# Kernel optimization log

Hardware: AMD Instinct MI355X
Metric: run time of the kernel (lower is better)

## Reference

```python
import jax, jax.numpy as jnp
import numpy as np

PAD_IDX = 0
VOCAB = 60
HIDDEN = 128
BATCH = 1024
SEQ = 256


def setup_inputs() -> dict:
    key = jax.random.key(0)
    ks = jax.random.split(key, 6)
    x = jax.random.randint(ks[0], (BATCH, SEQ), 0, VOCAB, dtype=jnp.int64 if jax.config.jax_enable_x64 else jnp.int32)
    lengths = jax.random.randint(ks[1], (BATCH,), 1, SEQ + 1, dtype=x.dtype)
    emb = jax.random.normal(ks[2], (VOCAB, HIDDEN), dtype=jnp.float32) * 0.1
    emb = emb.at[PAD_IDX].set(0.0)  # nn.Embedding padding_idx row is zero
    W_ih = jax.random.normal(ks[3], (HIDDEN, HIDDEN), dtype=jnp.float32) * (1.0 / np.sqrt(HIDDEN))
    W_hh = jax.random.normal(ks[4], (HIDDEN, HIDDEN), dtype=jnp.float32) * (1.0 / np.sqrt(HIDDEN))
    W_fc = jax.random.normal(ks[5], (VOCAB, HIDDEN), dtype=jnp.float32) * (1.0 / np.sqrt(HIDDEN))
    b_fc = jnp.zeros((VOCAB,), dtype=jnp.float32)
    return {"x": x, "lengths": lengths, "emb": emb, "W_ih": W_ih,
            "W_hh": W_hh, "W_fc": W_fc, "b_fc": b_fc}


def reference(x, lengths, emb, W_ih, W_hh, W_fc, b_fc):
    embedded = emb[x]                      # [B, T, H]
    B = embedded.shape[0]
    h0 = jnp.zeros((B, HIDDEN), dtype=embedded.dtype)

    def step(h_prev, x_t):
        # z_t = x_t @ W_ih^T + h_prev @ W_hh^T ; h_t = tanh(z_t)
        h_t = jnp.tanh(x_t @ W_ih.T + h_prev @ W_hh.T)
        return h_t, h_t

    _, hs = jax.lax.scan(step, h0, jnp.swapaxes(embedded, 0, 1))  # hs: [T, B, H]
    outputs = jnp.swapaxes(hs, 0, 1)       # [B, T, H]
    last_out = jnp.take_along_axis(outputs, (lengths - 1)[:, None, None], axis=1)[:, 0, :]  # [B, H]
    return last_out @ W_fc.T + b_fc[None, :]
```

## Files before the change

kernel.cpp:

```cpp
#include <hip/hip_runtime.h>
#include <hip/hip_bf16.h>

#define BATCH 1024
#define SEQ 256
#define HIDDEN 128
#define VOCAB 60
#define ROWS 4
#define CHUNK 16
#define ASTRIDE 144
#define RSTR 136

typedef _Float16 f16x8 __attribute__((ext_vector_type(8)));
typedef _Float16 f16x4 __attribute__((ext_vector_type(4)));
typedef float f32x4 __attribute__((ext_vector_type(4)));

__device__ __forceinline__ float fast_tanh(float x) {
    float e = __builtin_amdgcn_exp2f(x * 2.8853900817779268f);
    return __builtin_fmaf(-2.0f, __builtin_amdgcn_rcpf(e + 1.0f), 1.0f);
}

__global__ void rnn_prep_embw(const float* __restrict__ emb,
                              const float* __restrict__ W_ih,
                              float* __restrict__ embW) {
    const int v = blockIdx.x;
    const int i = threadIdx.x;
    __shared__ __align__(16) float e[HIDDEN];
    e[i] = emb[v * HIDDEN + i];
    __syncthreads();
    const float4* wrow = (const float4*)(W_ih + i * HIDDEN);
    const float4* e4 = (const float4*)e;
    float a0 = 0.f, a1 = 0.f, a2 = 0.f, a3 = 0.f;
#pragma unroll
    for (int j = 0; j < HIDDEN / 4; ++j) {
        float4 w = wrow[j];
        float4 h = e4[j];
        a0 += w.x * h.x; a1 += w.y * h.y; a2 += w.z * h.z; a3 += w.w * h.w;
    }
    embW[v * HIDDEN + i] = (a0 + a1) + (a2 + a3);
}

__global__ void __launch_bounds__(512)
rnn_mfma(const int* __restrict__ x, const int* __restrict__ lengths,
         const float* __restrict__ embW, const float* __restrict__ W_hh,
         const float* __restrict__ W_fc, const float* __restrict__ b_fc,
         float* __restrict__ out) {
    const int tid = threadIdx.x;
    const int wave = tid >> 6;
    const int lane = tid & 63;
    const int q = lane >> 4;
    const int r16 = lane & 15;
    const int r4 = r16 & 3;
    const int c0 = wave * 16;
    const int b0 = blockIdx.x * ROWS;

    __shared__ __align__(16) float ring[CHUNK][ROWS][RSTR];
    __shared__ __align__(16) _Float16 Ah[2][ROWS][ASTRIDE];
    __shared__ int xs[ROWS][SEQ + 1];
    __shared__ __align__(16) float hfin[ROWS][HIDDEN];
    __shared__ int lenbuf[ROWS];

    for (int idx = tid; idx < ROWS * SEQ; idx += 512) {
        int r = idx >> 8, t = idx & (SEQ - 1);
        xs[r][t] = x[(b0 + r) * SEQ + t];
    }
    if (tid < ROWS) lenbuf[tid] = lengths[b0 + tid];
    for (int idx = tid; idx < (int)(sizeof(Ah) / 4); idx += 512)
        ((int*)Ah)[idx] = 0;

    f16x8 Wf[4];
    {
        const float* wrow = W_hh + (c0 + r16) * HIDDEN + q * 8;
#pragma unroll
        for (int kc = 0; kc < 4; ++kc) {
            const float* p = wrow + kc * 32;
#pragma unroll
            for (int j = 0; j < 8; ++j) Wf[kc][j] = (_Float16)p[j];
        }
    }

    __syncthreads();

    const int mylen = lenbuf[r4];
    int lenmax = 0;
#pragma unroll
    for (int r = 0; r < ROWS; ++r) lenmax = max(lenmax, lenbuf[r]);

    const int s_c4 = tid & 31;
    const int s_r = (tid >> 5) & 3;
    const int s_tp = tid >> 7;

    f32x4 rg[4];
#pragma unroll
    for (int k = 0; k < 4; ++k) {
        int tp = s_tp + 4 * k;
        int tok = xs[s_r][tp];
        rg[k] = *(const f32x4*)(embW + tok * HIDDEN + s_c4 * 4);
    }

    int cur = 0;
    f32x4 cap = {0.f, 0.f, 0.f, 0.f};

    for (int t0 = 0; t0 < lenmax; t0 += CHUNK) {
#pragma unroll
        for (int k = 0; k < 4; ++k)
            *(f32x4*)&ring[s_tp + 4 * k][s_r][s_c4 * 4] = rg[k];
        __syncthreads();

        if (t0 + CHUNK < lenmax) {
            const int t0n = t0 + CHUNK;
#pragma unroll
            for (int k = 0; k < 4; ++k) {
                int tp = s_tp + 4 * k;
                int tok = xs[s_r][t0n + tp];
                rg[k] = *(const f32x4*)(embW + tok * HIDDEN + s_c4 * 4);
            }
        }

        const int tend = (lenmax - t0 < CHUNK) ? lenmax - t0 : CHUNK;
        for (int tt = 0; tt < tend; ++tt) {
            const _Float16* hb = &Ah[cur][r4][q * 8];
            f16x8 H0 = *(const f16x8*)(hb + 0);
            f16x8 H1 = *(const f16x8*)(hb + 32);
            f16x8 H2 = *(const f16x8*)(hb + 64);
            f16x8 H3 = *(const f16x8*)(hb + 96);

            f32x4 a = *(const f32x4*)&ring[tt][r4][c0 + 4 * q];
            f32x4 d = {0.f, 0.f, 0.f, 0.f};
            a = __builtin_amdgcn_mfma_f32_16x16x32_f16(Wf[0], H0, a, 0, 0, 0);
            d = __builtin_amdgcn_mfma_f32_16x16x32_f16(Wf[2], H2, d, 0, 0, 0);
            a = __builtin_amdgcn_mfma_f32_16x16x32_f16(Wf[1], H1, a, 0, 0, 0);
            d = __builtin_amdgcn_mfma_f32_16x16x32_f16(Wf[3], H3, d, 0, 0, 0);
            f32x4 z = a + d;

            f32x4 th;
            th[0] = fast_tanh(z[0]);
            th[1] = fast_tanh(z[1]);
            th[2] = fast_tanh(z[2]);
            th[3] = fast_tanh(z[3]);

            uint2 pk;
            pk.x = __builtin_bit_cast(unsigned int, __builtin_amdgcn_cvt_pkrtz(th[0], th[1]));
            pk.y = __builtin_bit_cast(unsigned int, __builtin_amdgcn_cvt_pkrtz(th[2], th[3]));

            const int nxt = cur ^ 1;
            if (r16 < ROWS)
                *(uint2*)&Ah[nxt][r16][c0 + 4 * q] = pk;
            if (t0 + tt + 1 == mylen) cap = th;
            __syncthreads();
            cur = nxt;
        }
    }

    if (r16 < ROWS)
        *(f32x4*)&hfin[r16][c0 + 4 * q] = cap;
    __syncthreads();

    const int r = tid >> 7;
    const int c = tid & 127;
    if (c < VOCAB) {
        const float4* hv = (const float4*)hfin[r];
        const float4* wf = (const float4*)(W_fc + c * HIDDEN);
        float a0 = 0.f, a1 = 0.f, a2 = 0.f, a3 = 0.f;
#pragma unroll
        for (int j = 0; j < HIDDEN / 4; ++j) {
            float4 h = hv[j];
            float4 w = wf[j];
            a0 += h.x * w.x; a1 += h.y * w.y; a2 += h.z * w.z; a3 += h.w * w.w;
        }
        out[(b0 + r) * VOCAB + c] = (a0 + a1) + (a2 + a3) + b_fc[c];
    }
}

extern "C" void kernel_launch(void* const* d_in, const int* in_sizes, int n_in,
                              void* d_out, int out_size, void* d_ws, size_t ws_size,
                              hipStream_t stream) {
    const int* x = (const int*)d_in[0];
    const int* lengths = (const int*)d_in[1];
    const float* emb = (const float*)d_in[2];
    const float* W_ih = (const float*)d_in[3];
    const float* W_hh = (const float*)d_in[4];
    const float* W_fc = (const float*)d_in[5];
    const float* b_fc = (const float*)d_in[6];
    float* out = (float*)d_out;

    float* embW = (float*)d_ws;

    rnn_prep_embw<<<VOCAB, HIDDEN, 0, stream>>>(emb, W_ih, embW);
    rnn_mfma<<<BATCH / ROWS, 512, 0, stream>>>(x, lengths, embW, W_hh, W_fc, b_fc, out);
}
```

Measured before the change: 160.6 us.

## Halve waves per block, give each wave two column tiles, prefetch embW directly

Each block now runs 4 waves instead of 8, and each wave computes two 16-column output tiles with 8 MFMAs per step. The shared-memory ring buffer and its chunked staging barrier are gone. Each lane instead loads its embW input-projection slice from global memory two timesteps ahead, in registers. The aim is to cut the cost of the per-step block barrier across fewer waves, raise per-wave MFMA work, and free LDS. The trade-off is more serial work per wave on the recurrent critical path and global-load latency that has to hide behind one step pair.

Result: slower. 176.7 us (+10.0%).

```diff
diff --git a/kernel.cpp b/kernel.cpp
--- a/kernel.cpp
+++ b/kernel.cpp
@@ -6,17 +6,19 @@
 #define HIDDEN 128
 #define VOCAB 60
 #define ROWS 4
-#define CHUNK 16
 #define ASTRIDE 144
-#define RSTR 136
+#define XSTR (SEQ + 4)
 
 typedef _Float16 f16x8 __attribute__((ext_vector_type(8)));
-typedef _Float16 f16x4 __attribute__((ext_vector_type(4)));
 typedef float f32x4 __attribute__((ext_vector_type(4)));
 
 __device__ __forceinline__ float fast_tanh(float x) {
     float e = __builtin_amdgcn_exp2f(x * 2.8853900817779268f);
     return __builtin_fmaf(-2.0f, __builtin_amdgcn_rcpf(e + 1.0f), 1.0f);
+}
+
+__device__ __forceinline__ f32x4 MF(f16x8 a, f16x8 b, f32x4 c) {
+    return __builtin_amdgcn_mfma_f32_16x16x32_f16(a, b, c, 0, 0, 0);
 }
 
 __global__ void rnn_prep_embw(const float* __restrict__ emb,
@@ -39,7 +41,7 @@
     embW[v * HIDDEN + i] = (a0 + a1) + (a2 + a3);
 }
 
-__global__ void __launch_bounds__(512)
+__global__ void __launch_bounds__(256)
 rnn_mfma(const int* __restrict__ x, const int* __restrict__ lengths,
          const float* __restrict__ embW, const float* __restrict__ W_hh,
          const float* __restrict__ W_fc, const float* __restrict__ b_fc,
@@ -50,124 +52,119 @@
     const int q = lane >> 4;
     const int r16 = lane & 15;
     const int r4 = r16 & 3;
-    const int c0 = wave * 16;
+    const int c0 = wave * 32;
     const int b0 = blockIdx.x * ROWS;
 
-    __shared__ __align__(16) float ring[CHUNK][ROWS][RSTR];
     __shared__ __align__(16) _Float16 Ah[2][ROWS][ASTRIDE];
-    __shared__ int xs[ROWS][SEQ + 1];
+    __shared__ __align__(16) int xs[ROWS][XSTR];
     __shared__ __align__(16) float hfin[ROWS][HIDDEN];
     __shared__ int lenbuf[ROWS];
 
-    for (int idx = tid; idx < ROWS * SEQ; idx += 512) {
+    for (int idx = tid; idx < ROWS * SEQ; idx += 256) {
         int r = idx >> 8, t = idx & (SEQ - 1);
         xs[r][t] = x[(b0 + r) * SEQ + t];
     }
     if (tid < ROWS) lenbuf[tid] = lengths[b0 + tid];
-    for (int idx = tid; idx < (int)(sizeof(Ah) / 4); idx += 512)
+    for (int idx = tid; idx < (int)(sizeof(Ah) / 4); idx += 256)
         ((int*)Ah)[idx] = 0;
 
-    f16x8 Wf[4];
-    {
-        const float* wrow = W_hh + (c0 + r16) * HIDDEN + q * 8;
+    f16x8 Wf[2][4];
+#pragma unroll
+    for (int cg = 0; cg < 2; ++cg) {
+        const float* wrow = W_hh + (c0 + cg * 16 + r16) * HIDDEN + q * 8;
 #pragma unroll
         for (int kc = 0; kc < 4; ++kc) {
             const float* p = wrow + kc * 32;
 #pragma unroll
-            for (int j = 0; j < 8; ++j) Wf[kc][j] = (_Float16)p[j];
+            for (int j = 0; j < 8; ++j) Wf[cg][kc][j] = (_Float16)p[j];
         }
     }
 
     __syncthreads();
 
     const int mylen = lenbuf[r4];
-    int lenmax = 0;
-#pragma unroll
-    for (int r = 0; r < ROWS; ++r) lenmax = max(lenmax, lenbuf[r]);
+    const int lenmax = max(max(lenbuf[0], lenbuf[1]), max(lenbuf[2], lenbuf[3]));
 
-    const int s_c4 = tid & 31;
-    const int s_r = (tid >> 5) & 3;
-    const int s_tp = tid >> 7;
+    const float* eb0 = embW + c0 + 4 * q;
 
-    f32x4 rg[4];
-#pragma unroll
-    for (int k = 0; k < 4; ++k) {
-        int tp = s_tp + 4 * k;
-        int tok = xs[s_r][tp];
-        rg[k] = *(const f32x4*)(embW + tok * HIDDEN + s_c4 * 4);
-    }
+    int2 tk = *(const int2*)&xs[r4][0];
+    f32x4 sa0 = *(const f32x4*)(eb0 + tk.x * HIDDEN);
+    f32x4 sb0 = *(const f32x4*)(eb0 + tk.x * HIDDEN + 16);
+    f32x4 sa1 = *(const f32x4*)(eb0 + tk.y * HIDDEN);
+    f32x4 sb1 = *(const f32x4*)(eb0 + tk.y * HIDDEN + 16);
 
     int cur = 0;
-    f32x4 cap = {0.f, 0.f, 0.f, 0.f};
+    f32x4 cap0 = {0.f, 0.f, 0.f, 0.f}, cap1 = {0.f, 0.f, 0.f, 0.f};
 
-    for (int t0 = 0; t0 < lenmax; t0 += CHUNK) {
-#pragma unroll
-        for (int k = 0; k < 4; ++k)
-            *(f32x4*)&ring[s_tp + 4 * k][s_r][s_c4 * 4] = rg[k];
-        __syncthreads();
+#define STEP(TT, SA, SB) do {                                              \
+    const _Float16* hb = &Ah[cur][r4][q * 8];                              \
+    f16x8 H0 = *(const f16x8*)(hb + 0);                                    \
+    f16x8 H1 = *(const f16x8*)(hb + 32);                                   \
+    f16x8 H2 = *(const f16x8*)(hb + 64);                                   \
+    f16x8 H3 = *(const f16x8*)(hb + 96);                                   \
+    f32x4 a0 = (SA), a1 = (SB);                                            \
+    f32x4 d0 = {0.f, 0.f, 0.f, 0.f}, d1 = {0.f, 0.f, 0.f, 0.f};            \
+    a0 = MF(Wf[0][0], H0, a0);  a1 = MF(Wf[1][0], H0, a1);                 \
+    d0 = MF(Wf[0][2], H2, d0);  d1 = MF(Wf[1][2], H2, d1);                 \
+    a0 = MF(Wf[0][1], H1, a0);  a1 = MF(Wf[1][1], H1, a1);                 \
+    d0 = MF(Wf[0][3], H3, d0);  d1 = MF(Wf[1][3], H3, d1);                 \
+    f32x4 z0 = a0 + d0, z1 = a1 + d1;                                      \
+    f32x4 th0, th1;                                                        \
+    th0[0] = fast_tanh(z0[0]); th0[1] = fast_tanh(z0[1]);                  \
+    th0[2] = fast_tanh(z0[2]); th0[3] = fast_tanh(z0[3]);                  \
+    th1[0] = fast_tanh(z1[0]); th1[1] = fast_tanh(z1[1]);                  \
+    th1[2] = fast_tanh(z1[2]); th1[3] = fast_tanh(z1[3]);                  \
+    uint2 p0, p1;                                                          \
+    p0.x = __builtin_bit_cast(unsigned int, __builtin_amdgcn_cvt_pkrtz(th0[0], th0[1])); \
+    p0.y = __builtin_bit_cast(unsigned int, __builtin_amdgcn_cvt_pkrtz(th0[2], th0[3])); \
+    p1.x = __builtin_bit_cast(unsigned int, __builtin_amdgcn_cvt_pkrtz(th1[0], th1[1])); \
+    p1.y = __builtin_bit_cast(unsigned int, __builtin_amdgcn_cvt_pkrtz(th1[2], th1[3])); \
+    const int nxt = cur ^ 1;                                               \
+    if (r16 < ROWS) {                  \
+        *(uint2*)&Ah[nxt][r16][c0 + 4 * q] = p0;                           \
+        *(uint2*)&Ah[nxt][r16][c0 + 16 + 4 * q] = p1;                      \
+    }                                                                      \
+    if ((TT) + 1 == mylen) { cap0 = th0; cap1 = th1; }                     \
+    __syncthreads();                                                       \
+    cur = nxt;                                                             \
+} while (0)
 
-        if (t0 + CHUNK < lenmax) {
-            const int t0n = t0 + CHUNK;
-#pragma unroll
-            for (int k = 0; k < 4; ++k) {
-                int tp = s_tp + 4 * k;
-                int tok = xs[s_r][t0n + tp];
-                rg[k] = *(const f32x4*)(embW + tok * HIDDEN + s_c4 * 4);
-            }
-        }
+    for (int t0 = 0; t0 < lenmax; t0 += 2) {
+        const int tb = min(t0 + 2, SEQ - 2);
+        int2 tkn = *(const int2*)&xs[r4][tb];
+        f32x4 na0 = *(const f32x4*)(eb0 + tkn.x * HIDDEN);
+        f32x4 nb0 = *(const f32x4*)(eb0 + tkn.x * HIDDEN + 16);
+        f32x4 na1 = *(const f32x4*)(eb0 + tkn.y * HIDDEN);
+        f32x4 nb1 = *(const f32x4*)(eb0 + tkn.y * HIDDEN + 16);
 
-        const int tend = (lenmax - t0 < CHUNK) ? lenmax - t0 : CHUNK;
-        for (int tt = 0; tt < tend; ++tt) {
-            const _Float16* hb = &Ah[cur][r4][q * 8];
-            f16x8 H0 = *(const f16x8*)(hb + 0);
-            f16x8 H1 = *(const f16x8*)(hb + 32);
-            f16x8 H2 = *(const f16x8*)(hb + 64);
-            f16x8 H3 = *(const f16x8*)(hb + 96);
+        STEP(t0, sa0, sb0);
+        STEP(t0 + 1, sa1, sb1);
 
-            f32x4 a = *(const f32x4*)&ring[tt][r4][c0 + 4 * q];
-            f32x4 d = {0.f, 0.f, 0.f, 0.f};
-            a = __builtin_amdgcn_mfma_f32_16x16x32_f16(Wf[0], H0, a, 0, 0, 0);
-            d = __builtin_amdgcn_mfma_f32_16x16x32_f16(Wf[2], H2, d, 0, 0, 0);
-            a = __builtin_amdgcn_mfma_f32_16x16x32_f16(Wf[1], H1, a, 0, 0, 0);
-            d = __builtin_amdgcn_mfma_f32_16x16x32_f16(Wf[3], H3, d, 0, 0, 0);
-            f32x4 z = a + d;
+        sa0 = na0; sb0 = nb0; sa1 = na1; sb1 = nb1;
+    }
+#undef STEP
 
-            f32x4 th;
-            th[0] = fast_tanh(z[0]);
-            th[1] = fast_tanh(z[1]);
-            th[2] = fast_tanh(z[2]);
-            th[3] = fast_tanh(z[3]);
-
-            uint2 pk;
-            pk.x = __builtin_bit_cast(unsigned int, __builtin_amdgcn_cvt_pkrtz(th[0], th[1]));
-            pk.y = __builtin_bit_cast(unsigned int, __builtin_amdgcn_cvt_pkrtz(th[2], th[3]));
-
-            const int nxt = cur ^ 1;
-            if (r16 < ROWS)
-                *(uint2*)&Ah[nxt][r16][c0 + 4 * q] = pk;
-            if (t0 + tt + 1 == mylen) cap = th;
-            __syncthreads();
-            cur = nxt;
-        }
+    if (r16 < ROWS) {
+        *(f32x4*)&hfin[r16][c0 + 4 * q] = cap0;
+        *(f32x4*)&hfin[r16][c0 + 16 + 4 * q] = cap1;
     }
-
-    if (r16 < ROWS)
-        *(f32x4*)&hfin[r16][c0 + 4 * q] = cap;
     __syncthreads();
 
-    const int r = tid >> 7;
-    const int c = tid & 127;
-    if (c < VOCAB) {
-        const float4* hv = (const float4*)hfin[r];
-        const float4* wf = (const float4*)(W_fc + c * HIDDEN);
-        float a0 = 0.f, a1 = 0.f, a2 = 0.f, a3 = 0.f;
+    for (int rc = tid; rc < ROWS * 128; rc += 256) {
+        const int r = rc >> 7;
+        const int c = rc & 127;
+        if (c < VOCAB) {
+            const float4* hv = (const float4*)hfin[r];
+            const float4* wf = (const float4*)(W_fc + c * HIDDEN);
+            float a0 = 0.f, a1 = 0.f, a2 = 0.f, a3 = 0.f;
 #pragma unroll
-        for (int j = 0; j < HIDDEN / 4; ++j) {
-            float4 h = hv[j];
-            float4 w = wf[j];
-            a0 += h.x * w.x; a1 += h.y * w.y; a2 += h.z * w.z; a3 += h.w * w.w;
+            for (int j = 0; j < HIDDEN / 4; ++j) {
+                float4 h = hv[j];
+                float4 w = wf[j];
+                a0 += h.x * w.x; a1 += h.y * w.y; a2 += h.z * w.z; a3 += h.w * w.w;
+            }
+            out[(b0 + r) * VOCAB + c] = (a0 + a1) + (a2 + a3) + b_fc[c];
         }
-        out[(b0 + r) * VOCAB + c] = (a0 + a1) + (a2 + a3) + b_fc[c];
     }
 }
 
@@ -186,5 +183,5 @@
     float* embW = (float*)d_ws;
 
     rnn_prep_embw<<<VOCAB, HIDDEN, 0, stream>>>(emb, W_ih, embW);
-    rnn_mfma<<<BATCH / ROWS, 512, 0, stream>>>(x, lengths, embW, W_hh, W_fc, b_fc, out);
+    rnn_mfma<<<BATCH / ROWS, 256, 0, stream>>>(x, lengths, embW, W_hh, W_fc, b_fc, out);
 }
```

## Interleave two independent batch groups per block to hide MFMA latency

Applied to the files above, without the earlier changes.

Each block now handles 8 batch rows as two independent 4-row recurrences that are processed in an interleaved way within each timestep. The goal is to fill MFMA and transcendental latency with independent work, and to cut the number of per-step barriers per row by half. The grid shrinks to 128 blocks, which leaves many CUs idle on a large GPU, and lenmax is now the maximum over 8 rows, so more padded steps run. The per-step barrier is replaced with an inline-asm lgkmcnt wait plus s_barrier.

New measurement: 244.4 us. 1.52x slower.

```diff
diff --git a/kernel.cpp b/kernel.cpp
--- a/kernel.cpp
+++ b/kernel.cpp
@@ -6,18 +6,26 @@
 #define HIDDEN 128
 #define VOCAB 60
 #define ROWS 4
+#define NPROB 2
+#define BROWS (ROWS*NPROB)
 #define CHUNK 16
 #define ASTRIDE 144
 #define RSTR 136
+#define XSTR 260
 
 typedef _Float16 f16x8 __attribute__((ext_vector_type(8)));
-typedef _Float16 f16x4 __attribute__((ext_vector_type(4)));
 typedef float f32x4 __attribute__((ext_vector_type(4)));
 
 __device__ __forceinline__ float fast_tanh(float x) {
     float e = __builtin_amdgcn_exp2f(x * 2.8853900817779268f);
     return __builtin_fmaf(-2.0f, __builtin_amdgcn_rcpf(e + 1.0f), 1.0f);
 }
+
+__device__ __forceinline__ f32x4 MF(f16x8 a, f16x8 b, f32x4 c) {
+    return __builtin_amdgcn_mfma_f32_16x16x32_f16(a, b, c, 0, 0, 0);
+}
+
+#define STEP_BARRIER() asm volatile("s_waitcnt lgkmcnt(0)\n\ts_barrier" ::: "memory")
 
 __global__ void rnn_prep_embw(const float* __restrict__ emb,
                               const float* __restrict__ W_ih,
@@ -51,19 +59,19 @@
     const int r16 = lane & 15;
     const int r4 = r16 & 3;
     const int c0 = wave * 16;
-    const int b0 = blockIdx.x * ROWS;
-
-    __shared__ __align__(16) float ring[CHUNK][ROWS][RSTR];
-    __shared__ __align__(16) _Float16 Ah[2][ROWS][ASTRIDE];
-    __shared__ int xs[ROWS][SEQ + 1];
-    __shared__ __align__(16) float hfin[ROWS][HIDDEN];
-    __shared__ int lenbuf[ROWS];
-
-    for (int idx = tid; idx < ROWS * SEQ; idx += 512) {
+    const int b0 = blockIdx.x * BROWS;
+
+    __shared__ __align__(16) float ring[NPROB][CHUNK][ROWS][RSTR];
+    __shared__ __align__(16) _Float16 Ah[NPROB][2][ROWS][ASTRIDE];
+    __shared__ __align__(16) int xs[BROWS][XSTR];
+    __shared__ __align__(16) float hfin[BROWS][HIDDEN];
+    __shared__ int lenbuf[BROWS];
+
+    for (int idx = tid; idx < BROWS * SEQ; idx += 512) {
         int r = idx >> 8, t = idx & (SEQ - 1);
         xs[r][t] = x[(b0 + r) * SEQ + t];
     }
-    if (tid < ROWS) lenbuf[tid] = lengths[b0 + tid];
+    if (tid < BROWS) lenbuf[tid] = lengths[b0 + tid];
     for (int idx = tid; idx < (int)(sizeof(Ah) / 4); idx += 512)
         ((int*)Ah)[idx] = 0;
 
@@ -80,83 +88,101 @@
 
     __syncthreads();
 
-    const int mylen = lenbuf[r4];
+    const int mylen0 = lenbuf[r4];
+    const int mylen1 = lenbuf[ROWS + r4];
     int lenmax = 0;
 #pragma unroll
-    for (int r = 0; r < ROWS; ++r) lenmax = max(lenmax, lenbuf[r]);
+    for (int r = 0; r < BROWS; ++r) lenmax = max(lenmax, lenbuf[r]);
 
     const int s_c4 = tid & 31;
     const int s_r = (tid >> 5) & 3;
     const int s_tp = tid >> 7;
 
-    f32x4 rg[4];
+    f32x4 rg0[4], rg1[4];
 #pragma unroll
     for (int k = 0; k < 4; ++k) {
         int tp = s_tp + 4 * k;
-        int tok = xs[s_r][tp];
-        rg[k] = *(const f32x4*)(embW + tok * HIDDEN + s_c4 * 4);
+        rg0[k] = *(const f32x4*)(embW + xs[s_r][tp] * HIDDEN + s_c4 * 4);
+        rg1[k] = *(const f32x4*)(embW + xs[ROWS + s_r][tp] * HIDDEN + s_c4 * 4);
     }
 
     int cur = 0;
-    f32x4 cap = {0.f, 0.f, 0.f, 0.f};
+    f32x4 cap0 = {0.f, 0.f, 0.f, 0.f}, cap1 = {0.f, 0.f, 0.f, 0.f};
 
     for (int t0 = 0; t0 < lenmax; t0 += CHUNK) {
 #pragma unroll
-        for (int k = 0; k < 4; ++k)
-            *(f32x4*)&ring[s_tp + 4 * k][s_r][s_c4 * 4] = rg[k];
+        for (int k = 0; k < 4; ++k) {
+            *(f32x4*)&ring[0][s_tp + 4 * k][s_r][s_c4 * 4] = rg0[k];
+            *(f32x4*)&ring[1][s_tp + 4 * k][s_r][s_c4 * 4] = rg1[k];
+        }
         __syncthreads();
 
         if (t0 + CHUNK < lenmax) {
             const int t0n = t0 + CHUNK;
 #pragma unroll
             for (int k = 0; k < 4; ++k) {
-                int tp = s_tp + 4 * k;
-                int tok = xs[s_r][t0n + tp];
-                rg[k] = *(const f32x4*)(embW + tok * HIDDEN + s_c4 * 4);
+                int tp = t0n + s_tp + 4 * k;
+                rg0[k] = *(const f32x4*)(embW + xs[s_r][tp] * HIDDEN + s_c4 * 4);
+                rg1[k] = *(const f32x4*)(embW + xs[ROWS + s_r][tp] * HIDDEN + s_c4 * 4);
             }
         }
 
         const int tend = (lenmax - t0 < CHUNK) ? lenmax - t0 : CHUNK;
         for (int tt = 0; tt < tend; ++tt) {
-            const _Float16* hb = &Ah[cur][r4][q * 8];
-            f16x8 H0 = *(const f16x8*)(hb + 0);
-            f16x8 H1 = *(const f16x8*)(hb + 32);
-            f16x8 H2 = *(const f16x8*)(hb + 64);
-            f16x8 H3 = *(const f16x8*)(hb + 96);
-
-            f32x4 a = *(const f32x4*)&ring[tt][r4][c0 + 4 * q];
-            f32x4 d = {0.f, 0.f, 0.f, 0.f};
-            a = __builtin_amdgcn_mfma_f32_16x16x32_f16(Wf[0], H0, a, 0, 0, 0);
-            d = __builtin_amdgcn_mfma_f32_16x16x32_f16(Wf[2], H2, d, 0, 0, 0);
-            a = __builtin_amdgcn_mfma_f32_16x16x32_f16(Wf[1], H1, a, 0, 0, 0);
-            d = __builtin_amdgcn_mfma_f32_16x16x32_f16(Wf[3], H3, d, 0, 0, 0);
-            f32x4 z = a + d;
-
-            f32x4 th;
-            th[0] = fast_tanh(z[0]);
-            th[1] = fast_tanh(z[1]);
-            th[2] = fast_tanh(z[2]);
-            th[3] = fast_tanh(z[3]);
-
-            uint2 pk;
-            pk.x = __builtin_bit_cast(unsigned int, __builtin_amdgcn_cvt_pkrtz(th[0], th[1]));
-            pk.y = __builtin_bit_cast(unsigned int, __builtin_amdgcn_cvt_pkrtz(th[2], th[3]));
+            const _Float16* hbA = &Ah[0][cur][r4][q * 8];
+            const _Float16* hbB = &Ah[1][cur][r4][q * 8];
+            f16x8 A0 = *(const f16x8*)(hbA + 0);
+            f16x8 A1 = *(const f16x8*)(hbA + 32);
+            f16x8 A2 = *(const f16x8*)(hbA + 64);
+            f16x8 A3 = *(const f16x8*)(hbA + 96);
+            f16x8 B0 = *(const f16x8*)(hbB + 0);
+            f16x8 B1 = *(const f16x8*)(hbB + 32);
+            f16x8 B2 = *(const f16x8*)(hbB + 64);
+            f16x8 B3 = *(const f16x8*)(hbB + 96);
+
+            f32x4 aA = *(const f32x4*)&ring[0][tt][r4][c0 + 4 * q];
+            f32x4 aB = *(const f32x4*)&ring[1][tt][r4][c0 + 4 * q];
+            f32x4 dA = {0.f, 0.f, 0.f, 0.f};
+            f32x4 dB = {0.f, 0.f, 0.f, 0.f};
+
+            aA = MF(Wf[0], A0, aA);  aB = MF(Wf[0], B0, aB);
+            dA = MF(Wf[2], A2, dA);  dB = MF(Wf[2], B2, dB);
+            aA = MF(Wf[1], A1, aA);  aB = MF(Wf[1], B1, aB);
+            dA = MF(Wf[3], A3, dA);  dB = MF(Wf[3], B3, dB);
+
+            f32x4 zA = aA + dA, zB = aB + dB;
+            f32x4 thA, thB;
+            thA[0] = fast_tanh(zA[0]); thB[0] = fast_tanh(zB[0]);
+            thA[1] = fast_tanh(zA[1]); thB[1] = fast_tanh(zB[1]);
+            thA[2] = fast_tanh(zA[2]); thB[2] = fast_tanh(zB[2]);
+            thA[3] = fast_tanh(zA[3]); thB[3] = fast_tanh(zB[3]);
+
+            uint2 pA, pB;
+            pA.x = __builtin_bit_cast(unsigned int, __builtin_amdgcn_cvt_pkrtz(thA[0], thA[1]));
+            pA.y = __builtin_bit_cast(unsigned int, __builtin_amdgcn_cvt_pkrtz(thA[2], thA[3]));
+            pB.x = __builtin_bit_cast(unsigned int, __builtin_amdgcn_cvt_pkrtz(thB[0], thB[1]));
+            pB.y = __builtin_bit_cast(unsigned int, __builtin_amdgcn_cvt_pkrtz(thB[2], thB[3]));
 
             const int nxt = cur ^ 1;
-            if (r16 < ROWS)
-                *(uint2*)&Ah[nxt][r16][c0 + 4 * q] = pk;
-            if (t0 + tt + 1 == mylen) cap = th;
-            __syncthreads();
+            if (r16 < ROWS) {
+                *(uint2*)&Ah[0][nxt][r16][c0 + 4 * q] = pA;
+                *(uint2*)&Ah[1][nxt][r16][c0 + 4 * q] = pB;
+            }
+            if (t0 + tt + 1 == mylen0) cap0 = thA;
+            if (t0 + tt + 1 == mylen1) cap1 = thB;
+            STEP_BARRIER();
             cur = nxt;
         }
     }
 
-    if (r16 < ROWS)
-        *(f32x4*)&hfin[r16][c0 + 4 * q] = cap;
+    if (r16 < ROWS) {
+        *(f32x4*)&hfin[r16][c0 + 4 * q] = cap0;
+        *(f32x4*)&hfin[ROWS + r16][c0 + 4 * q] = cap1;
+    }
     __syncthreads();
 
-    const int r = tid >> 7;
-    const int c = tid & 127;
+    const int r = tid >> 6;
+    const int c = tid & 63;
     if (c < VOCAB) {
         const float4* hv = (const float4*)hfin[r];
         const float4* wf = (const float4*)(W_fc + c * HIDDEN);
@@ -186,5 +212,5 @@
     float* embW = (float*)d_ws;
 
     rnn_prep_embw<<<VOCAB, HIDDEN, 0, stream>>>(emb, W_ih, embW);
-    rnn_mfma<<<BATCH / ROWS, 512, 0, stream>>>(x, lengths, embW, W_hh, W_fc, b_fc, out);
-}
+    rnn_mfma<<<BATCH / BROWS, 512, 0, stream>>>(x, lengths, embW, W_hh, W_fc, b_fc, out);
+}
```

## Give each wave a whole batch row to drop block barriers in recurrence

Applied to the files above, without the earlier changes.

Each wave now owns one batch row and holds all of W_hh in registers (32 f16x8 fragments), computing the full 128-wide hidden update with 32 MFMAs per step. No block-wide __syncthreads is needed per timestep, and each row runs only to its own length instead of the block maximum. The cost is much more MFMA work per row (the 16x16 tiles use only 1 of 16 batch columns), heavy register pressure, and one block per CU via launch bounds. Cross-lane hidden-state exchange through LDS within a wave now relies on implicit wave-level ordering.

Result: slower. 184.7 us (+15.0%).

```diff
diff --git a/kernel.cpp b/kernel.cpp
--- a/kernel.cpp
+++ b/kernel.cpp
@@ -1,22 +1,21 @@
 #include <hip/hip_runtime.h>
-#include <hip/hip_bf16.h>
 
 #define BATCH 1024
 #define SEQ 256
 #define HIDDEN 128
 #define VOCAB 60
-#define ROWS 4
-#define CHUNK 16
-#define ASTRIDE 144
-#define RSTR 136
+#define WPB 4
 
 typedef _Float16 f16x8 __attribute__((ext_vector_type(8)));
-typedef _Float16 f16x4 __attribute__((ext_vector_type(4)));
 typedef float f32x4 __attribute__((ext_vector_type(4)));
 
 __device__ __forceinline__ float fast_tanh(float x) {
     float e = __builtin_amdgcn_exp2f(x * 2.8853900817779268f);
     return __builtin_fmaf(-2.0f, __builtin_amdgcn_rcpf(e + 1.0f), 1.0f);
+}
+
+__device__ __forceinline__ f32x4 MF(f16x8 a, f16x8 b, f32x4 c) {
+    return __builtin_amdgcn_mfma_f32_16x16x32_f16(a, b, c, 0, 0, 0);
 }
 
 __global__ void rnn_prep_embw(const float* __restrict__ emb,
@@ -39,126 +38,102 @@
     embW[v * HIDDEN + i] = (a0 + a1) + (a2 + a3);
 }
 
-__global__ void __launch_bounds__(512)
-rnn_mfma(const int* __restrict__ x, const int* __restrict__ lengths,
-         const float* __restrict__ embW, const float* __restrict__ W_hh,
-         const float* __restrict__ W_fc, const float* __restrict__ b_fc,
-         float* __restrict__ out) {
+__global__ void __launch_bounds__(256, 1)
+rnn_wavelocal(const int* __restrict__ x, const int* __restrict__ lengths,
+              const float* __restrict__ embW, const float* __restrict__ W_hh,
+              const float* __restrict__ W_fc, const float* __restrict__ b_fc,
+              float* __restrict__ out) {
     const int tid = threadIdx.x;
     const int wave = tid >> 6;
     const int lane = tid & 63;
     const int q = lane >> 4;
-    const int r16 = lane & 15;
-    const int r4 = r16 & 3;
-    const int c0 = wave * 16;
-    const int b0 = blockIdx.x * ROWS;
+    const int n = lane & 15;
+    const int mg_own = n >> 1;
+    const int half = n & 1;
+    const int m_own = mg_own * 16 + q * 4 + half * 2;
+    const int row = blockIdx.x * WPB + wave;
 
-    __shared__ __align__(16) float ring[CHUNK][ROWS][RSTR];
-    __shared__ __align__(16) _Float16 Ah[2][ROWS][ASTRIDE];
-    __shared__ int xs[ROWS][SEQ + 1];
-    __shared__ __align__(16) float hfin[ROWS][HIDDEN];
-    __shared__ int lenbuf[ROWS];
+    __shared__ __align__(16) _Float16 hbuf[WPB][2][HIDDEN];
+    __shared__ __align__(16) float hf[WPB][HIDDEN];
 
-    for (int idx = tid; idx < ROWS * SEQ; idx += 512) {
-        int r = idx >> 8, t = idx & (SEQ - 1);
-        xs[r][t] = x[(b0 + r) * SEQ + t];
-    }
-    if (tid < ROWS) lenbuf[tid] = lengths[b0 + tid];
-    for (int idx = tid; idx < (int)(sizeof(Ah) / 4); idx += 512)
-        ((int*)Ah)[idx] = 0;
-
-    f16x8 Wf[4];
+    f16x8 Wf[8][4];
     {
-        const float* wrow = W_hh + (c0 + r16) * HIDDEN + q * 8;
+        const float* wr = W_hh + n * HIDDEN + q * 8;
 #pragma unroll
-        for (int kc = 0; kc < 4; ++kc) {
-            const float* p = wrow + kc * 32;
+        for (int mg = 0; mg < 8; ++mg) {
 #pragma unroll
-            for (int j = 0; j < 8; ++j) Wf[kc][j] = (_Float16)p[j];
+            for (int kc = 0; kc < 4; ++kc) {
+                const float* p = wr + mg * 16 * HIDDEN + kc * 32;
+                float4 w0 = *(const float4*)p;
+                float4 w1 = *(const float4*)(p + 4);
+                f16x8 f;
+                f[0] = (_Float16)w0.x; f[1] = (_Float16)w0.y;
+                f[2] = (_Float16)w0.z; f[3] = (_Float16)w0.w;
+                f[4] = (_Float16)w1.x; f[5] = (_Float16)w1.y;
+                f[6] = (_Float16)w1.z; f[7] = (_Float16)w1.w;
+                Wf[mg][kc] = f;
+            }
         }
     }
 
-    __syncthreads();
+    *(unsigned int*)&hbuf[wave][0][m_own] = 0u;
 
-    const int mylen = lenbuf[r4];
-    int lenmax = 0;
+    const int mylen = lengths[row];
+    const int* xrow = x + row * SEQ;
+
+    int tok0 = xrow[0];
+    int tok_nxt = xrow[1];
+    float2 sd_cur = *(const float2*)(embW + tok0 * HIDDEN + m_own);
+
+    float ta = 0.f, tb = 0.f;
+    int cur = 0;
+
+    for (int t = 0; t < mylen; ++t) {
+        float2 sd_nxt = *(const float2*)(embW + tok_nxt * HIDDEN + m_own);
+        int tok_n2 = xrow[(t + 2 < SEQ) ? t + 2 : SEQ - 1];
+
+        const _Float16* hb = &hbuf[wave][cur][q * 8];
+        f16x8 H0 = *(const f16x8*)(hb + 0);
+        f16x8 H1 = *(const f16x8*)(hb + 32);
+        f16x8 H2 = *(const f16x8*)(hb + 64);
+        f16x8 H3 = *(const f16x8*)(hb + 96);
+
+        const f32x4 Z = {0.f, 0.f, 0.f, 0.f};
+        f32x4 acc[8];
 #pragma unroll
-    for (int r = 0; r < ROWS; ++r) lenmax = max(lenmax, lenbuf[r]);
+        for (int mg = 0; mg < 8; ++mg) {
+            acc[mg] = MF(Wf[mg][0], H0, Z);
+            acc[mg] = MF(Wf[mg][1], H1, acc[mg]);
+            acc[mg] = MF(Wf[mg][2], H2, acc[mg]);
+            acc[mg] = MF(Wf[mg][3], H3, acc[mg]);
+        }
 
-    const int s_c4 = tid & 31;
-    const int s_r = (tid >> 5) & 3;
-    const int s_tp = tid >> 7;
+        float za = 0.f, zb = 0.f;
+#pragma unroll
+        for (int mg = 0; mg < 8; ++mg) {
+            za = (mg_own == mg) ? (half ? acc[mg][2] : acc[mg][0]) : za;
+            zb = (mg_own == mg) ? (half ? acc[mg][3] : acc[mg][1]) : zb;
+        }
 
-    f32x4 rg[4];
-#pragma unroll
-    for (int k = 0; k < 4; ++k) {
-        int tp = s_tp + 4 * k;
-        int tok = xs[s_r][tp];
-        rg[k] = *(const f32x4*)(embW + tok * HIDDEN + s_c4 * 4);
+        za += sd_cur.x;
+        zb += sd_cur.y;
+        ta = fast_tanh(za);
+        tb = fast_tanh(zb);
+
+        unsigned int pk = __builtin_bit_cast(unsigned int,
+                              __builtin_amdgcn_cvt_pkrtz(ta, tb));
+        const int nxt = cur ^ 1;
+        *(unsigned int*)&hbuf[wave][nxt][m_own] = pk;
+
+        sd_cur = sd_nxt;
+        tok_nxt = tok_n2;
+        cur = nxt;
     }
 
-    int cur = 0;
-    f32x4 cap = {0.f, 0.f, 0.f, 0.f};
-
-    for (int t0 = 0; t0 < lenmax; t0 += CHUNK) {
-#pragma unroll
-        for (int k = 0; k < 4; ++k)
-            *(f32x4*)&ring[s_tp + 4 * k][s_r][s_c4 * 4] = rg[k];
-        __syncthreads();
-
-        if (t0 + CHUNK < lenmax) {
-            const int t0n = t0 + CHUNK;
-#pragma unroll
-            for (int k = 0; k < 4; ++k) {
-                int tp = s_tp + 4 * k;
-                int tok = xs[s_r][t0n + tp];
-                rg[k] = *(const f32x4*)(embW + tok * HIDDEN + s_c4 * 4);
-            }
-        }
-
-        const int tend = (lenmax - t0 < CHUNK) ? lenmax - t0 : CHUNK;
-        for (int tt = 0; tt < tend; ++tt) {
-            const _Float16* hb = &Ah[cur][r4][q * 8];
-            f16x8 H0 = *(const f16x8*)(hb + 0);
-            f16x8 H1 = *(const f16x8*)(hb + 32);
-            f16x8 H2 = *(const f16x8*)(hb + 64);
-            f16x8 H3 = *(const f16x8*)(hb + 96);
-
-            f32x4 a = *(const f32x4*)&ring[tt][r4][c0 + 4 * q];
-            f32x4 d = {0.f, 0.f, 0.f, 0.f};
-            a = __builtin_amdgcn_mfma_f32_16x16x32_f16(Wf[0], H0, a, 0, 0, 0);
-            d = __builtin_amdgcn_mfma_f32_16x16x32_f16(Wf[2], H2, d, 0, 0, 0);
-            a = __builtin_amdgcn_mfma_f32_16x16x32_f16(Wf[1], H1, a, 0, 0, 0);
-            d = __builtin_amdgcn_mfma_f32_16x16x32_f16(Wf[3], H3, d, 0, 0, 0);
-            f32x4 z = a + d;
-
-            f32x4 th;
-            th[0] = fast_tanh(z[0]);
-            th[1] = fast_tanh(z[1]);
-            th[2] = fast_tanh(z[2]);
-            th[3] = fast_tanh(z[3]);
-
-            uint2 pk;
-            pk.x = __builtin_bit_cast(unsigned int, __builtin_amdgcn_cvt_pkrtz(th[0], th[1]));
-            pk.y = __builtin_bit_cast(unsigned int, __builtin_amdgcn_cvt_pkrtz(th[2], th[3]));
-
-            const int nxt = cur ^ 1;
-            if (r16 < ROWS)
-                *(uint2*)&Ah[nxt][r16][c0 + 4 * q] = pk;
-            if (t0 + tt + 1 == mylen) cap = th;
-            __syncthreads();
-            cur = nxt;
-        }
-    }
-
-    if (r16 < ROWS)
-        *(f32x4*)&hfin[r16][c0 + 4 * q] = cap;
-    __syncthreads();
-
-    const int r = tid >> 7;
-    const int c = tid & 127;
+    *(float2*)&hf[wave][m_own] = make_float2(ta, tb);
+    const int c = lane;
     if (c < VOCAB) {
-        const float4* hv = (const float4*)hfin[r];
+        const float4* hv = (const float4*)hf[wave];
         const float4* wf = (const float4*)(W_fc + c * HIDDEN);
         float a0 = 0.f, a1 = 0.f, a2 = 0.f, a3 = 0.f;
 #pragma unroll
@@ -167,7 +142,7 @@
             float4 w = wf[j];
             a0 += h.x * w.x; a1 += h.y * w.y; a2 += h.z * w.z; a3 += h.w * w.w;
         }
-        out[(b0 + r) * VOCAB + c] = (a0 + a1) + (a2 + a3) + b_fc[c];
+        out[row * VOCAB + c] = (a0 + a1) + (a2 + a3) + b_fc[c];
     }
 }
 
@@ -186,5 +161,6 @@
     float* embW = (float*)d_ws;
 
     rnn_prep_embw<<<VOCAB, HIDDEN, 0, stream>>>(emb, W_ih, embW);
-    rnn_mfma<<<BATCH / ROWS, 512, 0, stream>>>(x, lengths, embW, W_hh, W_fc, b_fc, out);
+    rnn_wavelocal<<<BATCH / WPB, 256, 0, stream>>>(x, lengths, embW, W_hh,
+                                                   W_fc, b_fc, out);
 }
```
